# Optimization experiments

Hardware: AMD Instinct MI355X
Metric: run time of the kernel (lower is better)

The kernel has to match this reference:

```python
import jax, jax.numpy as jnp
import numpy as np

N, NF, DIM, H, DH, DEPTH, EDIM, NB = 256, 127, 128, 8, 64, 6, 3, 512
INNER = H * DH  # 512
SCALE = DH ** -0.5
EPS = 1e-5


def setup_inputs() -> dict:
    key = jax.random.key(0)
    ks = jax.random.split(key, 16)
    p = lambda k, shape: jax.random.normal(k, shape, jnp.float32) * 0.02
    return {
        "coordinates": jax.random.normal(ks[0], (N, 3), jnp.float32),
        "bonds": jax.random.randint(ks[1], (NB, 2), 0, N),
        "noise_level": jax.random.uniform(ks[2], (1,), jnp.float32),
        "atom_emb": p(ks[3], (N, NF)),
        "ln1_g": jnp.ones((DEPTH, DIM)), "ln1_b": jnp.zeros((DEPTH, DIM)),
        "Wq": p(ks[4], (DEPTH, DIM, INNER)), "bq": jnp.zeros((DEPTH, INNER)),
        "Wkv": p(ks[5], (DEPTH, DIM, 2 * INNER)), "bkv": jnp.zeros((DEPTH, 2 * INNER)),
        "We": p(ks[6], (DEPTH, EDIM, INNER)), "be": jnp.zeros((DEPTH, INNER)),
        "Wo": p(ks[7], (DEPTH, INNER, DIM)), "bo": jnp.zeros((DEPTH, DIM)),
        "Wg1": p(ks[8], (DEPTH, 3 * DIM)),
        "ln2_g": jnp.ones((DEPTH, DIM)), "ln2_b": jnp.zeros((DEPTH, DIM)),
        "W1": p(ks[9], (DEPTH, DIM, 4 * DIM)), "b1": jnp.zeros((DEPTH, 4 * DIM)),
        "W2": p(ks[10], (DEPTH, 4 * DIM, DIM)), "b2": jnp.zeros((DEPTH, DIM)),
        "Wg2": p(ks[11], (DEPTH, 3 * DIM)),
        "out_w": p(ks[12], (DIM, 1)), "out_b": jnp.zeros((1,)),
    }


def _layernorm(x, g, b):
    m = jnp.mean(x, axis=-1, keepdims=True)
    v = jnp.mean((x - m) ** 2, axis=-1, keepdims=True)
    return (x - m) * jax.lax.rsqrt(v + EPS) * g + b


def _gated_residual(x, res, Wg):
    # Linear(3*dim -> 1, no bias) then sigmoid; mask is all-True so no masking.
    gate = jax.nn.sigmoid(jnp.concatenate([x, res, x - res], axis=-1) @ Wg)[..., None]
    return x * gate + res * (1.0 - gate)


def _forward(coordinates, bonds, noise_level, atom_emb, ln1_g, ln1_b, Wq, bq,
             Wkv, bkv, We, be, Wo, bo, Wg1, ln2_g, ln2_b, W1, b1, W2, b2, Wg2,
             out_w, out_b):
    n = coordinates.shape[0]
    # nodes: [n, NF] atom embeddings (looked up at arange(n)) + noise column -> [n, DIM]
    noise_col = jnp.broadcast_to(noise_level.reshape(1, 1), (n, 1))
    nodes = jnp.concatenate([atom_emb, noise_col], axis=-1)
    # dense edge tensor [n, n, 3]: coordinate differences at bonded pairs, antisymmetric
    bi, bj = bonds[:, 0], bonds[:, 1]
    diff = coordinates[bi] - coordinates[bj]
    edges = jnp.zeros((n, n, EDIM), jnp.float32).at[bi, bj].set(diff).at[bj, bi].set(-diff)

    for l in range(DEPTH):
        # --- edge-biased multi-head attention (PreNorm) ---
        x = _layernorm(nodes, ln1_g[l], ln1_b[l])
        q = (x @ Wq[l] + bq[l]).reshape(n, H, DH).transpose(1, 0, 2)          # [h, i, d]
        kv = x @ Wkv[l] + bkv[l]
        k = kv[:, :INNER].reshape(n, H, DH).transpose(1, 0, 2)                # [h, j, d]
        v = kv[:, INNER:].reshape(n, H, DH).transpose(1, 0, 2)                # [h, j, d]
        e = (edges @ We[l] + be[l]).reshape(n, n, H, DH).transpose(2, 0, 1, 3)  # [h, i, j, d]
        k_ij = k[:, None, :, :] + e                                            # [h, i, j, d]
        v_ij = v[:, None, :, :] + e
        sim = jnp.einsum('hid,hijd->hij', q, k_ij) * SCALE
        attn = jax.nn.softmax(sim, axis=-1)  # mask is all ones -> no-op
        out = jnp.einsum('hij,hijd->hid', attn, v_ij)                          # [h, i, d]
        out = out.transpose(1, 0, 2).reshape(n, INNER) @ Wo[l] + bo[l]         # [n, DIM]
        nodes = _gated_residual(out, nodes, Wg1[l])
        # --- feedforward (PreNorm) + gated residual ---
        y = _layernorm(nodes, ln2_g[l], ln2_b[l])
        y = jax.nn.gelu(y @ W1[l] + b1[l], approximate=False) @ W2[l] + b2[l]
        nodes = _gated_residual(y, nodes, Wg2[l])

    energy = nodes @ out_w + out_b  # [n, 1]
    return energy[None, :, :]       # [1, n, 1]


def reference(coordinates, bonds, noise_level, atom_emb, ln1_g, ln1_b, Wq, bq,
              Wkv, bkv, We, be, Wo, bo, Wg1, ln2_g, ln2_b, W1, b1, W2, b2, Wg2,
              out_w, out_b):
    return _forward(coordinates, bonds, noise_level, atom_emb, ln1_g, ln1_b,
                    Wq, bq, Wkv, bkv, We, be, Wo, bo, Wg1, ln2_g, ln2_b,
                    W1, b1, W2, b2, Wg2, out_w, out_b)
```

## Files before the change

kernel.cpp:

```cpp
#include <hip/hip_runtime.h>

#define NN     256
#define NF     127
#define DIM    128
#define NH     8
#define DH     64
#define INNER  512
#define DEPTH  6
#define NB     512
#define ATTN_SCALE 0.125f
#define LN_EPS 1e-5f

__device__ __forceinline__ float wred_sum(float v){
#pragma unroll
  for(int o=32;o;o>>=1) v += __shfl_xor(v,o);
  return v;
}
__device__ __forceinline__ float wred_max(float v){
#pragma unroll
  for(int o=32;o;o>>=1) v = fmaxf(v,__shfl_xor(v,o));
  return v;
}
__device__ __forceinline__ float block_sum(float v, float* sred, int t){
  v = wred_sum(v);
  __syncthreads();
  if((t&63)==0) sred[t>>6]=v;
  __syncthreads();
  float s = 0.f;
#pragma unroll
  for(int w=0; w<8; w++) s += sred[w];
  return s;
}

__device__ __forceinline__ void dev_ln(const float* in, float* out,
                                       const float* g, const float* b,
                                       float* sred, int t){
  float v = (t<DIM)? in[t] : 0.f;
  float m = block_sum(v,sred,t) * (1.f/DIM);
  float d = (t<DIM)? (v-m) : 0.f;
  float var = block_sum(d*d,sred,t) * (1.f/DIM);
  float rs = rsqrtf(var + LN_EPS);
  if(t<DIM) out[t] = d*rs*g[t] + b[t];
  __syncthreads();
}

__device__ __forceinline__ void dev_qkv4(const float* xs, int i,
    const float* Wq, const float* bq, const float* Wkv, const float* bkv,
    const float* be, float* qg, float* kT, float* vg, float* redS, int t){
  {
    const int cg4 = (t&127)*4, rq = t>>7;
    float4 acc = make_float4(0.f,0.f,0.f,0.f);
#pragma unroll
    for(int f=rq*32; f<rq*32+32; f++){
      float x = xs[f];
      float4 w = *(const float4*)(Wq + f*INNER + cg4);
      acc.x=fmaf(x,w.x,acc.x); acc.y=fmaf(x,w.y,acc.y);
      acc.z=fmaf(x,w.z,acc.z); acc.w=fmaf(x,w.w,acc.w);
    }
    *(float4*)(redS + rq*INNER + cg4) = acc;
  }
  __syncthreads();
  qg[i*INNER+t] = bq[t] + redS[t] + redS[INNER+t] + redS[2*INNER+t] + redS[3*INNER+t];
  __syncthreads();
  {
    const int cg4 = (t&255)*4, rh = t>>8;
    float4 acc = make_float4(0.f,0.f,0.f,0.f);
#pragma unroll 8
    for(int f=rh*64; f<rh*64+64; f++){
      float x = xs[f];
      float4 w = *(const float4*)(Wkv + f*(2*INNER) + cg4);
      acc.x=fmaf(x,w.x,acc.x); acc.y=fmaf(x,w.y,acc.y);
      acc.z=fmaf(x,w.z,acc.z); acc.w=fmaf(x,w.w,acc.w);
    }
    *(float4*)(redS + rh*(2*INNER) + cg4) = acc;
  }
  __syncthreads();
#pragma unroll
  for(int cc=0; cc<2; cc++){
    int c = t + cc*512;
    float s = redS[c] + redS[2*INNER+c] + bkv[c];
    if(c < INNER) kT[c*NN+i]          = s + be[c];
    else          vg[i*INNER+c-INNER] = s + be[c-INNER];
  }
  __syncthreads();
}

__global__ __launch_bounds__(512) void k_qkv0(const float* atom_emb, const float* noise,
    float* nodes,
    const float* ln1_g, const float* ln1_b,
    const float* Wq, const float* bq, const float* Wkv, const float* bkv, const float* be,
    float* qg, float* kT, float* vg){
  __shared__ float nd[DIM], xs[DIM], sred[8], redS[2048];
  int t = threadIdx.x, i = blockIdx.x;
  if(t<DIM){
    float v = (t<NF)? atom_emb[i*NF+t] : noise[0];
    nd[t] = v;
    nodes[i*DIM+t] = v;
  }
  __syncthreads();
  dev_ln(nd, xs, ln1_g, ln1_b, sred, t);
  dev_qkv4(xs, i, Wq, bq, Wkv, bkv, be, qg, kT, vg, redS, t);
}

__global__ __launch_bounds__(512) void k_layer(
    float* nodes, const float* qg, const float* kT, const float* vg,
    float* qg_n, float* kT_n, float* vg_n,
    const int* bonds, const float* coords,
    const float* We,
    const float* Wo, const float* bo, const float* Wg1,
    const float* ln2_g, const float* ln2_b,
    const float* W1, const float* b1, const float* W2, const float* b2,
    const float* Wg2,
    const float* ln1_g_n, const float* ln1_b_n,
    const float* Wq_n, const float* bq_n, const float* Wkv_n, const float* bkv_n,
    const float* be_n, int has_next)
{
  __shared__ float nd[DIM], xs[DIM], qs[INNER], ao[INNER], o128[DIM];
  __shared__ float eL[NN*3], aW[NH*NN], redS[2048], sred[8], qWe[NH*3];
  const int t = threadIdx.x, i = blockIdx.x;

  if(t<DIM) nd[t] = nodes[i*DIM+t];
  qs[t] = qg[i*INNER+t];
  eL[t] = 0.f;
  if(t<NN) eL[512+t] = 0.f;
  __syncthreads();

  {
    int bi = bonds[2*t], bj = bonds[2*t+1];
    if(bi==i || bj==i){
      float dx = coords[3*bi+0] - coords[3*bj+0];
      float dy = coords[3*bi+1] - coords[3*bj+1];
      float dz = coords[3*bi+2] - coords[3*bj+2];
      if(bi==i){ eL[bj*3+0]=dx;  eL[bj*3+1]=dy;  eL[bj*3+2]=dz;  }
      if(bj==i){ eL[bi*3+0]=-dx; eL[bi*3+1]=-dy; eL[bi*3+2]=-dz; }
    }
  }
  __syncthreads();

  if(t < NH*3){
    int h = t/3, c = t%3;
    float acc = 0.f;
    for(int d=0; d<DH; d++) acc = fmaf(qs[h*DH+d], We[c*INNER + h*DH + d], acc);
    qWe[t] = acc;
  }
  __syncthreads();

  {
    const int h = t>>6, l = t&63, j0 = 4*l;
    const float* kTh = kT + (h*DH)*NN;
    float s0=0.f,s1=0.f,s2=0.f,s3=0.f;
#pragma unroll 8
    for(int o=0; o<DH; o++){
      float qv = qs[h*DH+o];
      float4 kk = *(const float4*)(kTh + o*NN + j0);
      s0=fmaf(qv,kk.x,s0); s1=fmaf(qv,kk.y,s1); s2=fmaf(qv,kk.z,s2); s3=fmaf(qv,kk.w,s3);
    }
    float w0=qWe[h*3+0], w1=qWe[h*3+1], w2=qWe[h*3+2];
    s0 += w0*eL[(j0+0)*3+0] + w1*eL[(j0+0)*3+1] + w2*eL[(j0+0)*3+2];
    s1 += w0*eL[(j0+1)*3+0] + w1*eL[(j0+1)*3+1] + w2*eL[(j0+1)*3+2];
    s2 += w0*eL[(j0+2)*3+0] + w1*eL[(j0+2)*3+1] + w2*eL[(j0+2)*3+2];
    s3 += w0*eL[(j0+3)*3+0] + w1*eL[(j0+3)*3+1] + w2*eL[(j0+3)*3+2];
    s0*=ATTN_SCALE; s1*=ATTN_SCALE; s2*=ATTN_SCALE; s3*=ATTN_SCALE;
    float mx = wred_max(fmaxf(fmaxf(s0,s1),fmaxf(s2,s3)));
    float p0=expf(s0-mx), p1=expf(s1-mx), p2=expf(s2-mx), p3=expf(s3-mx);
    float inv = 1.f / wred_sum(p0+p1+p2+p3);
    float a0=p0*inv, a1=p1*inv, a2=p2*inv, a3=p3*inv;
    float* aw = aW + h*NN;
    *(float4*)(aw + j0) = make_float4(a0,a1,a2,a3);
    float c0 = a0*eL[(j0+0)*3+0]+a1*eL[(j0+1)*3+0]+a2*eL[(j0+2)*3+0]+a3*eL[(j0+3)*3+0];
    float c1 = a0*eL[(j0+0)*3+1]+a1*eL[(j0+1)*3+1]+a2*eL[(j0+2)*3+1]+a3*eL[(j0+3)*3+1];
    float c2 = a0*eL[(j0+0)*3+2]+a1*eL[(j0+1)*3+2]+a2*eL[(j0+2)*3+2]+a3*eL[(j0+3)*3+2];
    c0 = wred_sum(c0); c1 = wred_sum(c1); c2 = wred_sum(c2);
    __builtin_amdgcn_wave_barrier();
    const int dq = (l&15)*4, jg = l>>4;
    const float* vb = vg + h*DH + dq;
    float4 acc = make_float4(0.f,0.f,0.f,0.f);
#pragma unroll 8
    for(int jj=0; jj<64; jj++){
      int j = jg*64 + jj;
      float a = aw[j];
      float4 vv = *(const float4*)(vb + j*INNER);
      acc.x=fmaf(a,vv.x,acc.x); acc.y=fmaf(a,vv.y,acc.y);
      acc.z=fmaf(a,vv.z,acc.z); acc.w=fmaf(a,vv.w,acc.w);
    }
#pragma unroll
    for(int o=16;o<64;o<<=1){
      acc.x += __shfl_xor(acc.x,o); acc.y += __shfl_xor(acc.y,o);
      acc.z += __shfl_xor(acc.z,o); acc.w += __shfl_xor(acc.w,o);
    }
    if(l<16){
      float4 we0 = *(const float4*)(We + 0*INNER + h*DH + dq);
      float4 we1 = *(const float4*)(We + 1*INNER + h*DH + dq);
      float4 we2 = *(const float4*)(We + 2*INNER + h*DH + dq);
      float4 o;
      o.x = acc.x + c0*we0.x + c1*we1.x + c2*we2.x;
      o.y = acc.y + c0*we0.y + c1*we1.y + c2*we2.y;
      o.z = acc.z + c0*we0.z + c1*we1.z + c2*we2.z;
      o.w = acc.w + c0*we0.w + c1*we1.w + c2*we2.w;
      *(float4*)(ao + h*DH + dq) = o;
    }
  }
  __syncthreads();

  {
    const int cg4 = (t&31)*4, rg = t>>5;
    float4 acc = make_float4(0.f,0.f,0.f,0.f);
#pragma unroll
    for(int r=rg*32; r<rg*32+32; r++){
      float a = ao[r];
      float4 w = *(const float4*)(Wo + r*DIM + cg4);
      acc.x=fmaf(a,w.x,acc.x); acc.y=fmaf(a,w.y,acc.y);
      acc.z=fmaf(a,w.z,acc.z); acc.w=fmaf(a,w.w,acc.w);
    }
    *(float4*)(redS + rg*DIM + cg4) = acc;
    __syncthreads();
    if(t<DIM){
      float s = bo[t];
#pragma unroll
      for(int g=0; g<16; g++) s += redS[g*DIM+t];
      o128[t] = s;
    }
    __syncthreads();
    float gv = 0.f;
    if(t<DIM){
      float o = o128[t], r = nd[t];
      gv = o*Wg1[t] + r*Wg1[DIM+t] + (o-r)*Wg1[2*DIM+t];
    }
    float gs = block_sum(gv, sred, t);
    float gate = 1.f/(1.f + expf(-gs));
    if(t<DIM) nd[t] = o128[t]*gate + nd[t]*(1.f-gate);
    __syncthreads();
  }

  dev_ln(nd, xs, ln2_g, ln2_b, sred, t);
  {
    const int cg4 = (t&127)*4, rq = t>>7;
    float4 acc = make_float4(0.f,0.f,0.f,0.f);
#pragma unroll
    for(int f=rq*32; f<rq*32+32; f++){
      float x = xs[f];
      float4 w = *(const float4*)(W1 + f*INNER + cg4);
      acc.x=fmaf(x,w.x,acc.x); acc.y=fmaf(x,w.y,acc.y);
      acc.z=fmaf(x,w.z,acc.z); acc.w=fmaf(x,w.w,acc.w);
    }
    *(float4*)(redS + rq*INNER + cg4) = acc;
  }
  __syncthreads();
  {
    float a = b1[t] + redS[t] + redS[INNER+t] + redS[2*INNER+t] + redS[3*INNER+t];
    qs[t] = 0.5f*a*(1.f + erff(a*0.70710678118654752440f));
  }
  __syncthreads();
  {
    const int cg4 = (t&31)*4, rg = t>>5;
    float4 acc = make_float4(0.f,0.f,0.f,0.f);
#pragma unroll
    for(int m=rg*32; m<rg*32+32; m++){
      float a = qs[m];
      float4 w = *(const float4*)(W2 + m*DIM + cg4);
      acc.x=fmaf(a,w.x,acc.x); acc.y=fmaf(a,w.y,acc.y);
      acc.z=fmaf(a,w.z,acc.z); acc.w=fmaf(a,w.w,acc.w);
    }
    *(float4*)(redS + rg*DIM + cg4) = acc;
    __syncthreads();
    if(t<DIM){
      float s = b2[t];
#pragma unroll
      for(int g=0; g<16; g++) s += redS[g*DIM+t];
      o128[t] = s;
    }
    __syncthreads();
    float gv = 0.f;
    if(t<DIM){
      float y = o128[t], r = nd[t];
      gv = y*Wg2[t] + r*Wg2[DIM+t] + (y-r)*Wg2[2*DIM+t];
    }
    float gs = block_sum(gv, sred, t);
    float gate = 1.f/(1.f + expf(-gs));
    if(t<DIM) nd[t] = o128[t]*gate + nd[t]*(1.f-gate);
    __syncthreads();
  }
  if(t<DIM) nodes[i*DIM+t] = nd[t];

  if(has_next){
    dev_ln(nd, xs, ln1_g_n, ln1_b_n, sred, t);
    dev_qkv4(xs, i, Wq_n, bq_n, Wkv_n, bkv_n, be_n, qg_n, kT_n, vg_n, redS, t);
  }
}

__global__ __launch_bounds__(64) void k_energy(const float* nodes, const float* out_w,
                                               const float* out_b, float* out){
  int i = blockIdx.x, l = threadIdx.x;
  float a = fmaf(nodes[i*DIM+l], out_w[l], nodes[i*DIM+64+l]*out_w[64+l]);
  a = wred_sum(a);
  if(l==0) out[i] = a + out_b[0];
}

extern "C" void kernel_launch(void* const* d_in, const int* in_sizes, int n_in,
                              void* d_out, int out_size, void* d_ws, size_t ws_size,
                              hipStream_t stream){
  const float* coords   = (const float*)d_in[0];
  const int*   bonds    = (const int*  )d_in[1];
  const float* noise    = (const float*)d_in[2];
  const float* atom_emb = (const float*)d_in[3];
  const float* ln1_g = (const float*)d_in[4];
  const float* ln1_b = (const float*)d_in[5];
  const float* Wq    = (const float*)d_in[6];
  const float* bq    = (const float*)d_in[7];
  const float* Wkv   = (const float*)d_in[8];
  const float* bkv   = (const float*)d_in[9];
  const float* We    = (const float*)d_in[10];
  const float* be    = (const float*)d_in[11];
  const float* Wo    = (const float*)d_in[12];
  const float* bo    = (const float*)d_in[13];
  const float* Wg1   = (const float*)d_in[14];
  const float* ln2_g = (const float*)d_in[15];
  const float* ln2_b = (const float*)d_in[16];
  const float* W1    = (const float*)d_in[17];
  const float* b1    = (const float*)d_in[18];
  const float* W2    = (const float*)d_in[19];
  const float* b2    = (const float*)d_in[20];
  const float* Wg2   = (const float*)d_in[21];
  const float* out_w = (const float*)d_in[22];
  const float* out_b = (const float*)d_in[23];

  float* ws = (float*)d_ws;
  float* nodes   = ws;
  float* qbuf[2] = { ws +  32768, ws + 163840 };
  float* kbuf[2] = { ws + 294912, ws + 425984 };
  float* vbuf[2] = { ws + 557056, ws + 688128 };

  k_qkv0<<<256, 512, 0, stream>>>(atom_emb, noise, nodes, ln1_g, ln1_b,
                                  Wq, bq, Wkv, bkv, be,
                                  qbuf[0], kbuf[0], vbuf[0]);
  for(int l=0; l<DEPTH; l++){
    int cur = l&1, nxt = cur^1;
    int has_next = (l < DEPTH-1);
    int ln = has_next ? l+1 : l;
    k_layer<<<256, 512, 0, stream>>>(
      nodes, qbuf[cur], kbuf[cur], vbuf[cur],
      qbuf[nxt], kbuf[nxt], vbuf[nxt],
      bonds, coords,
      We  + (size_t)l*3*INNER,
      Wo  + (size_t)l*INNER*DIM, bo + (size_t)l*DIM, Wg1 + (size_t)l*3*DIM,
      ln2_g + (size_t)l*DIM, ln2_b + (size_t)l*DIM,
      W1  + (size_t)l*DIM*4*DIM, b1 + (size_t)l*4*DIM,
      W2  + (size_t)l*4*DIM*DIM, b2 + (size_t)l*DIM, Wg2 + (size_t)l*3*DIM,
      ln1_g + (size_t)ln*DIM, ln1_b + (size_t)ln*DIM,
      Wq  + (size_t)ln*DIM*INNER, bq + (size_t)ln*INNER,
      Wkv + (size_t)ln*DIM*2*INNER, bkv + (size_t)ln*2*INNER,
      be  + (size_t)ln*INNER, has_next);
  }
  k_energy<<<256, 64, 0, stream>>>(nodes, out_w, out_b, (float*)d_out);
}
```

Measured before the change: 320.2 us.

## Replace block reductions with redundant per-wave LN/gate and fold energy into last layer

Every wave now holds the node vector in registers and computes LayerNorm and gate reductions redundantly with wave shuffles, which removes the block_sum shared-memory barriers. Edge features move to a structure-of-arrays layout for float4 loads, and the qWe projection is computed with shuffles instead of a serial 24-thread loop. The final energy projection is fused into the last layer launch, so the separate energy kernel is gone. LayerNorm variance switches to E[x^2]-m^2, which is slightly less stable numerically. The V-loop index is staggered per lane group to reduce LDS bank conflicts.

```diff
diff --git a/kernel.cpp b/kernel.cpp
--- a/kernel.cpp
+++ b/kernel.cpp
@@ -11,6 +11,9 @@
 #define ATTN_SCALE 0.125f
 #define LN_EPS 1e-5f
 
+#define FMA4(A_, S_, V_) { A_.x=fmaf(S_,(V_).x,A_.x); A_.y=fmaf(S_,(V_).y,A_.y); \
+                           A_.z=fmaf(S_,(V_).z,A_.z); A_.w=fmaf(S_,(V_).w,A_.w); }
+
 __device__ __forceinline__ float wred_sum(float v){
 #pragma unroll
   for(int o=32;o;o>>=1) v += __shfl_xor(v,o);
@@ -21,85 +24,106 @@
   for(int o=32;o;o>>=1) v = fmaxf(v,__shfl_xor(v,o));
   return v;
 }
-__device__ __forceinline__ float block_sum(float v, float* sred, int t){
-  v = wred_sum(v);
-  __syncthreads();
-  if((t&63)==0) sred[t>>6]=v;
-  __syncthreads();
-  float s = 0.f;
-#pragma unroll
-  for(int w=0; w<8; w++) s += sred[w];
-  return s;
-}
-
-__device__ __forceinline__ void dev_ln(const float* in, float* out,
-                                       const float* g, const float* b,
-                                       float* sred, int t){
-  float v = (t<DIM)? in[t] : 0.f;
-  float m = block_sum(v,sred,t) * (1.f/DIM);
-  float d = (t<DIM)? (v-m) : 0.f;
-  float var = block_sum(d*d,sred,t) * (1.f/DIM);
+__device__ __forceinline__ float2 wred_sum2(float a, float b){
+#pragma unroll
+  for(int o=32;o;o>>=1){ a += __shfl_xor(a,o); b += __shfl_xor(b,o); }
+  return make_float2(a,b);
+}
+
+__device__ __forceinline__ void ln_wave(float n0, float n1,
+                                        const float* g, const float* b, int l,
+                                        float& x0, float& x1){
+  float2 sv = wred_sum2(n0+n1, n0*n0+n1*n1);
+  float m  = sv.x*(1.f/DIM);
+  float var = sv.y*(1.f/DIM) - m*m;
   float rs = rsqrtf(var + LN_EPS);
-  if(t<DIM) out[t] = d*rs*g[t] + b[t];
-  __syncthreads();
-}
-
-__device__ __forceinline__ void dev_qkv4(const float* xs, int i,
+  x0 = (n0-m)*rs*g[l]    + b[l];
+  x1 = (n1-m)*rs*g[64+l] + b[64+l];
+}
+
+__device__ __forceinline__ void gate_wave(float o0, float o1, float& n0, float& n1,
+                                          const float* Wg, int l){
+  float gv = o0*Wg[l]    + n0*Wg[DIM+l]    + (o0-n0)*Wg[2*DIM+l]
+           + o1*Wg[64+l] + n1*Wg[DIM+64+l] + (o1-n1)*Wg[2*DIM+64+l];
+  gv = wred_sum(gv);
+  float gate = 1.f/(1.f + expf(-gv));
+  n0 = o0*gate + n0*(1.f-gate);
+  n1 = o1*gate + n1*(1.f-gate);
+}
+
+__device__ __forceinline__ void mvp128_512(const float* xin, const float* W,
+                                           float* SC, int t){
+  const int cg4 = (t&127)<<2, fq = t>>7;
+  float4 acc = make_float4(0.f,0.f,0.f,0.f);
+#pragma unroll 8
+  for(int f=fq*32; f<fq*32+32; f++){
+    float4 wv = *(const float4*)(W + f*INNER + cg4);
+    float xv = xin[f];
+    FMA4(acc, xv, wv);
+  }
+  *(float4*)(SC + fq*INNER + cg4) = acc;
+}
+
+__device__ __forceinline__ void mvp128_1024(const float* xin, const float* W,
+                                            float* SC, int t){
+  const int cg4 = (t&255)<<2, rh = t>>8;
+  float4 acc = make_float4(0.f,0.f,0.f,0.f);
+#pragma unroll 8
+  for(int f=rh*64; f<rh*64+64; f++){
+    float4 wv = *(const float4*)(W + f*(2*INNER) + cg4);
+    float xv = xin[f];
+    FMA4(acc, xv, wv);
+  }
+  *(float4*)(SC + rh*(2*INNER) + cg4) = acc;
+}
+
+__device__ __forceinline__ void mvp512_128(const float* ain, const float* W,
+                                           float* SC, int t){
+  const int cg4 = (t&31)<<2, fg = t>>5;
+  float4 acc = make_float4(0.f,0.f,0.f,0.f);
+#pragma unroll 8
+  for(int f=fg*32; f<fg*32+32; f++){
+    float4 wv = *(const float4*)(W + f*DIM + cg4);
+    float av = ain[f];
+    FMA4(acc, av, wv);
+  }
+  *(float4*)(SC + fg*DIM + cg4) = acc;
+}
+
+__device__ __forceinline__ void qkv_tail(const float* xs, int i,
     const float* Wq, const float* bq, const float* Wkv, const float* bkv,
-    const float* be, float* qg, float* kT, float* vg, float* redS, int t){
-  {
-    const int cg4 = (t&127)*4, rq = t>>7;
-    float4 acc = make_float4(0.f,0.f,0.f,0.f);
-#pragma unroll
-    for(int f=rq*32; f<rq*32+32; f++){
-      float x = xs[f];
-      float4 w = *(const float4*)(Wq + f*INNER + cg4);
-      acc.x=fmaf(x,w.x,acc.x); acc.y=fmaf(x,w.y,acc.y);
-      acc.z=fmaf(x,w.z,acc.z); acc.w=fmaf(x,w.w,acc.w);
-    }
-    *(float4*)(redS + rq*INNER + cg4) = acc;
-  }
-  __syncthreads();
-  qg[i*INNER+t] = bq[t] + redS[t] + redS[INNER+t] + redS[2*INNER+t] + redS[3*INNER+t];
-  __syncthreads();
-  {
-    const int cg4 = (t&255)*4, rh = t>>8;
-    float4 acc = make_float4(0.f,0.f,0.f,0.f);
-#pragma unroll 8
-    for(int f=rh*64; f<rh*64+64; f++){
-      float x = xs[f];
-      float4 w = *(const float4*)(Wkv + f*(2*INNER) + cg4);
-      acc.x=fmaf(x,w.x,acc.x); acc.y=fmaf(x,w.y,acc.y);
-      acc.z=fmaf(x,w.z,acc.z); acc.w=fmaf(x,w.w,acc.w);
-    }
-    *(float4*)(redS + rh*(2*INNER) + cg4) = acc;
-  }
+    const float* be, float* qgn, float* kTn, float* vgn, float* SC, int t){
+  mvp128_512(xs, Wq, SC, t);
+  __syncthreads();
+  qgn[i*INNER + t] = bq[t] + SC[t] + SC[INNER+t] + SC[2*INNER+t] + SC[3*INNER+t];
+  __syncthreads();
+  mvp128_1024(xs, Wkv, SC, t);
   __syncthreads();
 #pragma unroll
   for(int cc=0; cc<2; cc++){
     int c = t + cc*512;
-    float s = redS[c] + redS[2*INNER+c] + bkv[c];
-    if(c < INNER) kT[c*NN+i]          = s + be[c];
-    else          vg[i*INNER+c-INNER] = s + be[c-INNER];
-  }
-  __syncthreads();
+    float s = bkv[c] + SC[c] + SC[2*INNER+c];
+    if(c < INNER) kTn[c*NN + i]            = s + be[c];
+    else          vgn[i*INNER + c - INNER] = s + be[c-INNER];
+  }
 }
 
 __global__ __launch_bounds__(512) void k_qkv0(const float* atom_emb, const float* noise,
-    float* nodes,
-    const float* ln1_g, const float* ln1_b,
+    float* nodes, const float* ln1_g, const float* ln1_b,
     const float* Wq, const float* bq, const float* Wkv, const float* bkv, const float* be,
     float* qg, float* kT, float* vg){
-  __shared__ float nd[DIM], xs[DIM], sred[8], redS[2048];
-  int t = threadIdx.x, i = blockIdx.x;
-  if(t<DIM){
-    float v = (t<NF)? atom_emb[i*NF+t] : noise[0];
-    nd[t] = v;
-    nodes[i*DIM+t] = v;
-  }
-  __syncthreads();
-  dev_ln(nd, xs, ln1_g, ln1_b, sred, t);
-  dev_qkv4(xs, i, Wq, bq, Wkv, bkv, be, qg, kT, vg, redS, t);
+  __shared__ __align__(16) float SC[2048];
+  __shared__ __align__(16) float xsm[DIM];
+  const int t = threadIdx.x, i = blockIdx.x;
+  const int w = t>>6, l = t&63;
+  float nd0 = (l<NF)?      atom_emb[i*NF + l]      : noise[0];
+  float nd1 = (64+l<NF)?   atom_emb[i*NF + 64 + l] : noise[0];
+  if(w==0){ nodes[i*DIM + l] = nd0; nodes[i*DIM + 64 + l] = nd1; }
+  float x0, x1;
+  ln_wave(nd0, nd1, ln1_g, ln1_b, l, x0, x1);
+  xsm[l] = x0; xsm[64+l] = x1;
+  __syncthreads();
+  qkv_tail(xsm, i, Wq, bq, Wkv, bkv, be, qg, kT, vg, SC, t);
 }
 
 __global__ __launch_bounds__(512) void k_layer(
@@ -113,75 +137,83 @@
     const float* Wg2,
     const float* ln1_g_n, const float* ln1_b_n,
     const float* Wq_n, const float* bq_n, const float* Wkv_n, const float* bkv_n,
-    const float* be_n, int has_next)
+    const float* be_n,
+    const float* out_w, const float* out_b, float* eout, int has_next)
 {
-  __shared__ float nd[DIM], xs[DIM], qs[INNER], ao[INNER], o128[DIM];
-  __shared__ float eL[NN*3], aW[NH*NN], redS[2048], sred[8], qWe[NH*3];
+  __shared__ __align__(16) float SC[2048];
+  __shared__ __align__(16) float qs[INNER];
+  __shared__ __align__(16) float ao[INNER];
+  __shared__ __align__(16) float eb[3*NN];
+  __shared__ __align__(16) float xsm[DIM];
   const int t = threadIdx.x, i = blockIdx.x;
-
-  if(t<DIM) nd[t] = nodes[i*DIM+t];
-  qs[t] = qg[i*INNER+t];
-  eL[t] = 0.f;
-  if(t<NN) eL[512+t] = 0.f;
-  __syncthreads();
-
-  {
-    int bi = bonds[2*t], bj = bonds[2*t+1];
+  const int w = t>>6, l = t&63;
+
+  qs[t] = qg[i*INNER + t];
+  eb[t&511] = 0.f;
+  if(t < 256) eb[512 + t] = 0.f;
+  float nd0 = nodes[i*DIM + l];
+  float nd1 = nodes[i*DIM + 64 + l];
+  __syncthreads();
+
+  {
+    const int bi = bonds[2*t], bj = bonds[2*t+1];
     if(bi==i || bj==i){
       float dx = coords[3*bi+0] - coords[3*bj+0];
       float dy = coords[3*bi+1] - coords[3*bj+1];
       float dz = coords[3*bi+2] - coords[3*bj+2];
-      if(bi==i){ eL[bj*3+0]=dx;  eL[bj*3+1]=dy;  eL[bj*3+2]=dz;  }
-      if(bj==i){ eL[bi*3+0]=-dx; eL[bi*3+1]=-dy; eL[bi*3+2]=-dz; }
-    }
-  }
-  __syncthreads();
-
-  if(t < NH*3){
-    int h = t/3, c = t%3;
-    float acc = 0.f;
-    for(int d=0; d<DH; d++) acc = fmaf(qs[h*DH+d], We[c*INNER + h*DH + d], acc);
-    qWe[t] = acc;
-  }
-  __syncthreads();
-
-  {
-    const int h = t>>6, l = t&63, j0 = 4*l;
-    const float* kTh = kT + (h*DH)*NN;
+      if(bi==i){ eb[bj]=dx;  eb[NN+bj]=dy;  eb[2*NN+bj]=dz;  }
+      if(bj==i){ eb[bi]=-dx; eb[NN+bi]=-dy; eb[2*NN+bi]=-dz; }
+    }
+  }
+  __syncthreads();
+
+  {
+    const int h = w, j0 = l<<2, qb = h*DH;
+    float qwe0, qwe1, qwe2;
+    {
+      float qv = qs[qb + l];
+      qwe0 = qv*We[0*INNER + qb + l];
+      qwe1 = qv*We[1*INNER + qb + l];
+      qwe2 = qv*We[2*INNER + qb + l];
+#pragma unroll
+      for(int o=32;o;o>>=1){
+        qwe0 += __shfl_xor(qwe0,o); qwe1 += __shfl_xor(qwe1,o); qwe2 += __shfl_xor(qwe2,o);
+      }
+    }
+    const float* kTh = kT + qb*NN;
     float s0=0.f,s1=0.f,s2=0.f,s3=0.f;
 #pragma unroll 8
-    for(int o=0; o<DH; o++){
-      float qv = qs[h*DH+o];
+    for(int o=0;o<DH;o++){
+      float qv = qs[qb + o];
       float4 kk = *(const float4*)(kTh + o*NN + j0);
       s0=fmaf(qv,kk.x,s0); s1=fmaf(qv,kk.y,s1); s2=fmaf(qv,kk.z,s2); s3=fmaf(qv,kk.w,s3);
     }
-    float w0=qWe[h*3+0], w1=qWe[h*3+1], w2=qWe[h*3+2];
-    s0 += w0*eL[(j0+0)*3+0] + w1*eL[(j0+0)*3+1] + w2*eL[(j0+0)*3+2];
-    s1 += w0*eL[(j0+1)*3+0] + w1*eL[(j0+1)*3+1] + w2*eL[(j0+1)*3+2];
-    s2 += w0*eL[(j0+2)*3+0] + w1*eL[(j0+2)*3+1] + w2*eL[(j0+2)*3+2];
-    s3 += w0*eL[(j0+3)*3+0] + w1*eL[(j0+3)*3+1] + w2*eL[(j0+3)*3+2];
-    s0*=ATTN_SCALE; s1*=ATTN_SCALE; s2*=ATTN_SCALE; s3*=ATTN_SCALE;
+    float4 ex = *(const float4*)(eb + j0);
+    float4 ey = *(const float4*)(eb + NN + j0);
+    float4 ez = *(const float4*)(eb + 2*NN + j0);
+    s0 = (s0 + qwe0*ex.x + qwe1*ey.x + qwe2*ez.x)*ATTN_SCALE;
+    s1 = (s1 + qwe0*ex.y + qwe1*ey.y + qwe2*ez.y)*ATTN_SCALE;
+    s2 = (s2 + qwe0*ex.z + qwe1*ey.z + qwe2*ez.z)*ATTN_SCALE;
+    s3 = (s3 + qwe0*ex.w + qwe1*ey.w + qwe2*ez.w)*ATTN_SCALE;
     float mx = wred_max(fmaxf(fmaxf(s0,s1),fmaxf(s2,s3)));
     float p0=expf(s0-mx), p1=expf(s1-mx), p2=expf(s2-mx), p3=expf(s3-mx);
     float inv = 1.f / wred_sum(p0+p1+p2+p3);
     float a0=p0*inv, a1=p1*inv, a2=p2*inv, a3=p3*inv;
-    float* aw = aW + h*NN;
-    *(float4*)(aw + j0) = make_float4(a0,a1,a2,a3);
-    float c0 = a0*eL[(j0+0)*3+0]+a1*eL[(j0+1)*3+0]+a2*eL[(j0+2)*3+0]+a3*eL[(j0+3)*3+0];
-    float c1 = a0*eL[(j0+0)*3+1]+a1*eL[(j0+1)*3+1]+a2*eL[(j0+2)*3+1]+a3*eL[(j0+3)*3+1];
-    float c2 = a0*eL[(j0+0)*3+2]+a1*eL[(j0+1)*3+2]+a2*eL[(j0+2)*3+2]+a3*eL[(j0+3)*3+2];
+    *(float4*)(SC + h*NN + j0) = make_float4(a0,a1,a2,a3);
+    float c0 = a0*ex.x + a1*ex.y + a2*ex.z + a3*ex.w;
+    float c1 = a0*ey.x + a1*ey.y + a2*ey.z + a3*ey.w;
+    float c2 = a0*ez.x + a1*ez.y + a2*ez.z + a3*ez.w;
     c0 = wred_sum(c0); c1 = wred_sum(c1); c2 = wred_sum(c2);
     __builtin_amdgcn_wave_barrier();
-    const int dq = (l&15)*4, jg = l>>4;
-    const float* vb = vg + h*DH + dq;
+    const int dq = (l&15)<<2, jg = l>>4;
+    const float* vb = vg + qb + dq;
     float4 acc = make_float4(0.f,0.f,0.f,0.f);
 #pragma unroll 8
-    for(int jj=0; jj<64; jj++){
-      int j = jg*64 + jj;
-      float a = aw[j];
+    for(int jj=0;jj<64;jj++){
+      int j = (jg<<6) + ((jj + (jg<<3)) & 63);
+      float a = SC[h*NN + j];
       float4 vv = *(const float4*)(vb + j*INNER);
-      acc.x=fmaf(a,vv.x,acc.x); acc.y=fmaf(a,vv.y,acc.y);
-      acc.z=fmaf(a,vv.z,acc.z); acc.w=fmaf(a,vv.w,acc.w);
+      FMA4(acc, a, vv);
     }
 #pragma unroll
     for(int o=16;o<64;o<<=1){
@@ -189,111 +221,61 @@
       acc.z += __shfl_xor(acc.z,o); acc.w += __shfl_xor(acc.w,o);
     }
     if(l<16){
-      float4 we0 = *(const float4*)(We + 0*INNER + h*DH + dq);
-      float4 we1 = *(const float4*)(We + 1*INNER + h*DH + dq);
-      float4 we2 = *(const float4*)(We + 2*INNER + h*DH + dq);
-      float4 o;
-      o.x = acc.x + c0*we0.x + c1*we1.x + c2*we2.x;
-      o.y = acc.y + c0*we0.y + c1*we1.y + c2*we2.y;
-      o.z = acc.z + c0*we0.z + c1*we1.z + c2*we2.z;
-      o.w = acc.w + c0*we0.w + c1*we1.w + c2*we2.w;
-      *(float4*)(ao + h*DH + dq) = o;
-    }
-  }
-  __syncthreads();
-
-  {
-    const int cg4 = (t&31)*4, rg = t>>5;
-    float4 acc = make_float4(0.f,0.f,0.f,0.f);
-#pragma unroll
-    for(int r=rg*32; r<rg*32+32; r++){
-      float a = ao[r];
-      float4 w = *(const float4*)(Wo + r*DIM + cg4);
-      acc.x=fmaf(a,w.x,acc.x); acc.y=fmaf(a,w.y,acc.y);
-      acc.z=fmaf(a,w.z,acc.z); acc.w=fmaf(a,w.w,acc.w);
-    }
-    *(float4*)(redS + rg*DIM + cg4) = acc;
+      float4 we0 = *(const float4*)(We + 0*INNER + qb + dq);
+      float4 we1 = *(const float4*)(We + 1*INNER + qb + dq);
+      float4 we2 = *(const float4*)(We + 2*INNER + qb + dq);
+      float4 ov;
+      ov.x = acc.x + c0*we0.x + c1*we1.x + c2*we2.x;
+      ov.y = acc.y + c0*we0.y + c1*we1.y + c2*we2.y;
+      ov.z = acc.z + c0*we0.z + c1*we1.z + c2*we2.z;
+      ov.w = acc.w + c0*we0.w + c1*we1.w + c2*we2.w;
+      *(float4*)(ao + qb + dq) = ov;
+    }
+  }
+  __syncthreads();
+
+  mvp512_128(ao, Wo, SC, t);
+  __syncthreads();
+  {
+    float o0 = bo[l], o1 = bo[64+l];
+#pragma unroll
+    for(int fg=0; fg<16; fg++){ o0 += SC[fg*DIM + l]; o1 += SC[fg*DIM + 64 + l]; }
+    gate_wave(o0, o1, nd0, nd1, Wg1, l);
+    float x0, x1;
+    ln_wave(nd0, nd1, ln2_g, ln2_b, l, x0, x1);
+    xsm[l] = x0; xsm[64+l] = x1;
+  }
+  __syncthreads();
+
+  mvp128_512(xsm, W1, SC, t);
+  __syncthreads();
+  {
+    float a = b1[t] + SC[t] + SC[INNER+t] + SC[2*INNER+t] + SC[3*INNER+t];
+    qs[t] = 0.5f*a*(1.f + erff(a*0.70710678118654752440f));
+  }
+  __syncthreads();
+  mvp512_128(qs, W2, SC, t);
+  __syncthreads();
+  {
+    float y0 = b2[l], y1 = b2[64+l];
+#pragma unroll
+    for(int fg=0; fg<16; fg++){ y0 += SC[fg*DIM + l]; y1 += SC[fg*DIM + 64 + l]; }
+    gate_wave(y0, y1, nd0, nd1, Wg2, l);
+    if(w==0){ nodes[i*DIM + l] = nd0; nodes[i*DIM + 64 + l] = nd1; }
+    if(has_next){
+      float x0, x1;
+      ln_wave(nd0, nd1, ln1_g_n, ln1_b_n, l, x0, x1);
+      xsm[l] = x0; xsm[64+l] = x1;
+    } else if(w==0){
+      float ev = nd0*out_w[l] + nd1*out_w[64+l];
+      ev = wred_sum(ev);
+      if(l==0) eout[i] = ev + out_b[0];
+    }
+  }
+  if(has_next){
     __syncthreads();
-    if(t<DIM){
-      float s = bo[t];
-#pragma unroll
-      for(int g=0; g<16; g++) s += redS[g*DIM+t];
-      o128[t] = s;
-    }
-    __syncthreads();
-    float gv = 0.f;
-    if(t<DIM){
-      float o = o128[t], r = nd[t];
-      gv = o*Wg1[t] + r*Wg1[DIM+t] + (o-r)*Wg1[2*DIM+t];
-    }
-    float gs = block_sum(gv, sred, t);
-    float gate = 1.f/(1.f + expf(-gs));
-    if(t<DIM) nd[t] = o128[t]*gate + nd[t]*(1.f-gate);
-    __syncthreads();
-  }
-
-  dev_ln(nd, xs, ln2_g, ln2_b, sred, t);
-  {
-    const int cg4 = (t&127)*4, rq = t>>7;
-    float4 acc = make_float4(0.f,0.f,0.f,0.f);
-#pragma unroll
-    for(int f=rq*32; f<rq*32+32; f++){
-      float x = xs[f];
-      float4 w = *(const float4*)(W1 + f*INNER + cg4);
-      acc.x=fmaf(x,w.x,acc.x); acc.y=fmaf(x,w.y,acc.y);
-      acc.z=fmaf(x,w.z,acc.z); acc.w=fmaf(x,w.w,acc.w);
-    }
-    *(float4*)(redS + rq*INNER + cg4) = acc;
-  }
-  __syncthreads();
-  {
-    float a = b1[t] + redS[t] + redS[INNER+t] + redS[2*INNER+t] + redS[3*INNER+t];
-    qs[t] = 0.5f*a*(1.f + erff(a*0.70710678118654752440f));
-  }
-  __syncthreads();
-  {
-    const int cg4 = (t&31)*4, rg = t>>5;
-    float4 acc = make_float4(0.f,0.f,0.f,0.f);
-#pragma unroll
-    for(int m=rg*32; m<rg*32+32; m++){
-      float a = qs[m];
-      float4 w = *(const float4*)(W2 + m*DIM + cg4);
-      acc.x=fmaf(a,w.x,acc.x); acc.y=fmaf(a,w.y,acc.y);
-      acc.z=fmaf(a,w.z,acc.z); acc.w=fmaf(a,w.w,acc.w);
-    }
-    *(float4*)(redS + rg*DIM + cg4) = acc;
-    __syncthreads();
-    if(t<DIM){
-      float s = b2[t];
-#pragma unroll
-      for(int g=0; g<16; g++) s += redS[g*DIM+t];
-      o128[t] = s;
-    }
-    __syncthreads();
-    float gv = 0.f;
-    if(t<DIM){
-      float y = o128[t], r = nd[t];
-      gv = y*Wg2[t] + r*Wg2[DIM+t] + (y-r)*Wg2[2*DIM+t];
-    }
-    float gs = block_sum(gv, sred, t);
-    float gate = 1.f/(1.f + expf(-gs));
-    if(t<DIM) nd[t] = o128[t]*gate + nd[t]*(1.f-gate);
-    __syncthreads();
-  }
-  if(t<DIM) nodes[i*DIM+t] = nd[t];
-
-  if(has_next){
-    dev_ln(nd, xs, ln1_g_n, ln1_b_n, sred, t);
-    dev_qkv4(xs, i, Wq_n, bq_n, Wkv_n, bkv_n, be_n, qg_n, kT_n, vg_n, redS, t);
-  }
-}
-
-__global__ __launch_bounds__(64) void k_energy(const float* nodes, const float* out_w,
-                                               const float* out_b, float* out){
-  int i = blockIdx.x, l = threadIdx.x;
-  float a = fmaf(nodes[i*DIM+l], out_w[l], nodes[i*DIM+64+l]*out_w[64+l]);
-  a = wred_sum(a);
-  if(l==0) out[i] = a + out_b[0];
+    qkv_tail(xsm, i, Wq_n, bq_n, Wkv_n, bkv_n, be_n, qg_n, kT_n, vg_n, SC, t);
+  }
 }
 
 extern "C" void kernel_launch(void* const* d_in, const int* in_sizes, int n_in,
@@ -330,14 +312,14 @@
   float* kbuf[2] = { ws + 294912, ws + 425984 };
   float* vbuf[2] = { ws + 557056, ws + 688128 };
 
-  k_qkv0<<<256, 512, 0, stream>>>(atom_emb, noise, nodes, ln1_g, ln1_b,
-                                  Wq, bq, Wkv, bkv, be,
-                                  qbuf[0], kbuf[0], vbuf[0]);
+  k_qkv0<<<NN, 512, 0, stream>>>(atom_emb, noise, nodes, ln1_g, ln1_b,
+                                 Wq, bq, Wkv, bkv, be,
+                                 qbuf[0], kbuf[0], vbuf[0]);
   for(int l=0; l<DEPTH; l++){
     int cur = l&1, nxt = cur^1;
     int has_next = (l < DEPTH-1);
     int ln = has_next ? l+1 : l;
-    k_layer<<<256, 512, 0, stream>>>(
+    k_layer<<<NN, 512, 0, stream>>>(
       nodes, qbuf[cur], kbuf[cur], vbuf[cur],
       qbuf[nxt], kbuf[nxt], vbuf[nxt],
       bonds, coords,
@@ -349,7 +331,7 @@
       ln1_g + (size_t)ln*DIM, ln1_b + (size_t)ln*DIM,
       Wq  + (size_t)ln*DIM*INNER, bq + (size_t)ln*INNER,
       Wkv + (size_t)ln*DIM*2*INNER, bkv + (size_t)ln*2*INNER,
-      be  + (size_t)ln*INNER, has_next);
-  }
-  k_energy<<<256, 64, 0, stream>>>(nodes, out_w, out_b, (float*)d_out);
-}
+      be  + (size_t)ln*INNER,
+      out_w, out_b, (float*)d_out, has_next);
+  }
+}
```

Result: faster. 304.9 us (-4.8%).
